# Performance work log

Hardware: AMD Instinct MI355X
Metric: run time of the kernel (lower is better)

## Reference

```python
import jax, jax.numpy as jnp
import numpy as np

B, L, D, K = 16, 2048, 128, 8192
NUM_RQ_STEPS = 1


def _nearest(residual, codebook):
    # residual: [B,L,D], codebook: [K,D]
    d2 = (
        jnp.sum(residual * residual, axis=-1, keepdims=True)  # [B,L,1]
        - 2.0 * jnp.einsum('bld,kd->blk', residual, codebook)  # [B,L,K]
        + jnp.sum(codebook * codebook, axis=-1)  # [K]
    )
    idx = jnp.argmin(d2, axis=-1)  # [B,L]
    return codebook[idx], idx  # gather: [B,L,D]


def setup_inputs() -> dict:
    key = jax.random.key(0)
    k1, k2 = jax.random.split(key)
    z_e = jax.random.normal(k1, (B, L, D), dtype=jnp.float32)
    codebook = jax.random.normal(k2, (K, D), dtype=jnp.float32)
    return {"z_e": z_e, "codebook": codebook}


def reference(z_e, codebook):
    # apply_codebook(z_e, code_sg=True): codebook is stop-gradiented,
    # residual quantization over NUM_RQ_STEPS, straight-through on output.
    cb = jax.lax.stop_gradient(codebook)
    residual = z_e
    z_q = jnp.zeros_like(z_e)
    idx_list = []
    for _ in range(NUM_RQ_STEPS):
        q, idx = _nearest(residual, cb)
        z_q = z_q + q
        residual = residual - q
        idx_list.append(idx)
    indices = jnp.stack(idx_list, axis=-1)  # [B,L,num_rq_steps]
    # straight-through estimator (code_sg=True): grads flow to z_e, not codebook
    z_q = z_e + jax.lax.stop_gradient(z_q - z_e)
    return z_q, indices
```

## Files before the change

### kernel.cpp

```cpp
#include <hip/hip_runtime.h>


#define M_TOK  32768
#define DIM    128
#define KCODES 8192
#define BM     64
#define NT     (KCODES / 256)
#define MARGIN 0.10f
#define RTG    8

typedef _Float16 half8v __attribute__((ext_vector_type(8)));
typedef float float4v __attribute__((ext_vector_type(4)));

union H2U { _Float16 h; unsigned short u; };
__device__ __forceinline__ unsigned short f2h_bits(_Float16 h) {
  H2U c; c.h = h; return c.u;
}

__device__ __forceinline__ void gload_lds16(const void* g, void* l) {
  __builtin_amdgcn_global_load_lds(
      (const __attribute__((address_space(1))) unsigned int*)g,
      (__attribute__((address_space(3))) unsigned int*)l, 16, 0, 0);
}

#define CONSUME_SLICE(P, CNTTXT)                                       \
  do {                                                                 \
    asm volatile("s_waitcnt vmcnt(" CNTTXT ")" ::: "memory");          \
    __builtin_amdgcn_sched_barrier(0);                                 \
    half8v bf[4];                                                      \
    _Pragma("unroll") for (int j_ = 0; j_ < 4; ++j_)                   \
      bf[j_] = *(const half8v*)(BsW + (P) * 4096 + boff[j_]);          \
    _Pragma("unroll") for (int i_ = 0; i_ < 4; ++i_)                   \
      _Pragma("unroll") for (int j_ = 0; j_ < 4; ++j_)                 \
        acc[i_][j_] = __builtin_amdgcn_mfma_f32_16x16x32_f16(          \
            ahi[P][i_], bf[j_], acc[i_][j_], 0, 0, 0);                 \
  } while (0)

#define CNORM_OFF  (KCODES * 256)
#define QCNT_OFF   (CNORM_OFF + KCODES * 4)
#define QTOK_OFF   (QCNT_OFF + 64)
#define KMIN_OFF   (QTOK_OFF + M_TOK * 4)

__global__ __launch_bounds__(256) void prep_kernel(
    const float* __restrict__ cb, unsigned short* __restrict__ Cs,
    float* __restrict__ cnorm, int* __restrict__ qcnt) {
  if (blockIdx.x == 0 && threadIdx.x == 0) *qcnt = 0;
  const int k = blockIdx.x * 4 + (threadIdx.x >> 6);
  const int lane = threadIdx.x & 63;
  const float2 v = ((const float2*)(cb + (size_t)k * DIM))[lane];
  float s = v.x * v.x + v.y * v.y;
  #pragma unroll
  for (int off = 32; off > 0; off >>= 1) s += __shfl_down(s, off);
  if (lane == 0) cnorm[k] = s;
  ushort2 hi;
  hi.x = f2h_bits((_Float16)v.x);
  hi.y = f2h_bits((_Float16)v.y);
  *(ushort2*)(Cs + (size_t)k * 128 + lane * 2) = hi;
}

__global__ __launch_bounds__(256, 2) void vq_mfma_kernel(
    const float* __restrict__ ze, const unsigned short* __restrict__ Cs,
    const float* __restrict__ cnorm, const float* __restrict__ cb,
    int* __restrict__ qcnt, int* __restrict__ qtok,
    unsigned long long* __restrict__ kmin,
    float* __restrict__ out_zq, float* __restrict__ out_idx) {
  __shared__ char lds[65536];
  char* const As = lds;

  const int tid = threadIdx.x;
  const int wn = tid >> 6;
  const int lane = tid & 63;
  const int quad = lane >> 4;
  const int l15 = lane & 15;
  const int m0 = blockIdx.x * BM;

  int loffC[4];
  #pragma unroll
  for (int c = 0; c < 4; ++c) {
    const int r = c * 16 + (lane >> 2);
    const int s = lane & 3;
    const int seg = s ^ ((r >> 1) & 3);
    loffC[c] = (wn * 64 + r) * 256 + seg * 16;
  }
  int boff[4];
  #pragma unroll
  for (int j = 0; j < 4; ++j) {
    const int n = j * 16 + l15;
    boff[j] = n * 64 + ((quad ^ ((n >> 1) & 3)) << 4);
  }
  char* const BsW = lds + wn * 16384;

  {
    const int r = tid >> 2;
    const int qh = tid & 3;
    const float* zrow = ze + (size_t)(m0 + r) * DIM + qh * 32;
    char* arow = As + r * 256;
    const int rx = r & 7;
    #pragma unroll
    for (int i = 0; i < 8; ++i) {
      const float4 v = *(const float4*)(zrow + i * 4);
      ushort4 hh;
      hh.x = f2h_bits((_Float16)v.x);
      hh.y = f2h_bits((_Float16)v.y);
      hh.z = f2h_bits((_Float16)v.z);
      hh.w = f2h_bits((_Float16)v.w);
      const int c = qh * 32 + i * 4;
      *(ushort4*)(arow + ((((c >> 3) ^ rx) << 4) | ((c & 7) << 1))) = hh;
    }
  }
  __syncthreads();

  half8v ahi[4][4];
  #pragma unroll
  for (int ks = 0; ks < 4; ++ks)
    #pragma unroll
    for (int i = 0; i < 4; ++i) {
      const int m = i * 16 + l15;
      const int kslot = ks * 4 + quad;
      ahi[ks][i] = *(const half8v*)(As + m * 256 + ((kslot ^ (m & 7)) << 4));
    }
  __syncthreads();

  float bestv[16], secv[16], idxv[16];
  #pragma unroll
  for (int s = 0; s < 16; ++s) {
    bestv[s] = -3.4e38f; secv[s] = -3.4e38f; idxv[s] = 0.f;
  }

  for (int nt = 0; nt < NT; ++nt) {
    const char* const tile = (const char*)Cs + (size_t)nt * 65536;
    float cnv[4];
    #pragma unroll
    for (int j = 0; j < 4; ++j)
      cnv[j] = cnorm[nt * 256 + wn * 64 + j * 16 + l15];

    float4v acc[4][4];
    #pragma unroll
    for (int i = 0; i < 4; ++i)
      #pragma unroll
      for (int j = 0; j < 4; ++j) acc[i][j] = (float4v)0.0f;

    asm volatile("s_waitcnt lgkmcnt(0)" ::: "memory");
    __builtin_amdgcn_sched_barrier(0);
    #pragma unroll
    for (int p = 0; p < 4; ++p)
      #pragma unroll
      for (int c = 0; c < 4; ++c)
        gload_lds16(tile + p * 64 + loffC[c], BsW + p * 4096 + c * 1024);

    CONSUME_SLICE(0, "12");
    CONSUME_SLICE(1, "8");
    CONSUME_SLICE(2, "4");
    CONSUME_SLICE(3, "0");

    #pragma unroll
    for (int j = 0; j < 4; ++j) {
      const float nidx = (float)(nt * 256 + wn * 64 + j * 16 + l15);
      const float cn = cnv[j];
      #pragma unroll
      for (int i = 0; i < 4; ++i)
        #pragma unroll
        for (int rg = 0; rg < 4; ++rg) {
          const float sc = fmaf(-0.5f, cn, acc[i][j][rg]);
          const int slot = i * 4 + rg;
          const bool bt = sc > bestv[slot];
          secv[slot] = __builtin_amdgcn_fmed3f(sc, bestv[slot], secv[slot]);
          idxv[slot] = bt ? nidx : idxv[slot];
          bestv[slot] = fmaxf(bestv[slot], sc);
        }
    }
  }

  #pragma unroll
  for (int slot = 0; slot < 16; ++slot) {
    float b = bestv[slot], sec = secv[slot], ix = idxv[slot];
    #pragma unroll
    for (int mk = 1; mk <= 8; mk <<= 1) {
      const float ob = __shfl_xor(b, mk);
      const float os = __shfl_xor(sec, mk);
      const float oi = __shfl_xor(ix, mk);
      const bool take = (ob > b) || (ob == b && oi < ix);
      const float loser = take ? b : ob;
      b = take ? ob : b;
      ix = take ? oi : ix;
      sec = fmaxf(fmaxf(sec, os), loser);
    }
    bestv[slot] = b; secv[slot] = sec; idxv[slot] = ix;
  }

  __syncthreads();
  float* const redB = (float*)lds;
  float* const redS = redB + 256;
  float* const redI = redB + 512;
  float* const lidxs = redB + 768;
  if (l15 == 0) {
    #pragma unroll
    for (int slot = 0; slot < 16; ++slot) {
      const int row = (slot >> 2) * 16 + quad * 4 + (slot & 3);
      redB[wn * 64 + row] = bestv[slot];
      redS[wn * 64 + row] = secv[slot];
      redI[wn * 64 + row] = idxv[slot];
    }
  }
  __syncthreads();
  if (tid < 64) {
    float b = redB[tid], sec = redS[tid], ix = redI[tid];
    #pragma unroll
    for (int w = 1; w < 4; ++w) {
      const float ob = redB[w * 64 + tid];
      const float os = redS[w * 64 + tid];
      const float oi = redI[w * 64 + tid];
      const bool take = (ob > b) || (ob == b && oi < ix);
      const float loser = take ? b : ob;
      b = take ? ob : b;
      ix = take ? oi : ix;
      sec = fmaxf(fmaxf(sec, os), loser);
    }
    out_idx[m0 + tid] = ix;
    lidxs[tid] = ix;
    if (b - sec < 0.5f * MARGIN) {
      kmin[m0 + tid] = ~0ull;
      const int p = atomicAdd(qcnt, 1);
      qtok[p] = m0 + tid;
    }
  }
  __syncthreads();

  const int tl = tid >> 2, qp = tid & 3;
  const int code = (int)lidxs[tl];
  const float4* src = (const float4*)(cb + (size_t)code * DIM);
  float4* dst = (float4*)(out_zq + (size_t)(m0 + tl) * DIM);
  #pragma unroll
  for (int p = 0; p < 8; ++p) dst[qp + p * 4] = src[qp + p * 4];
}

__global__ __launch_bounds__(256) void rescan_part_kernel(
    const float* __restrict__ ze, const float* __restrict__ cb,
    const float* __restrict__ cnorm, const int* __restrict__ qcnt,
    const int* __restrict__ qtok, unsigned long long* __restrict__ kmin) {
  __shared__ float xsh[RTG][132];
  __shared__ unsigned long long wpart[4][RTG];
  const int tid = threadIdx.x;
  const int wv = tid >> 6;
  const int lane = tid & 63;
  const int cg = blockIdx.x & 7;
  const int n = *qcnt;
  const int nslots = gridDim.x >> 3;
  const int c0 = cg * 1024 + tid;

  for (int g = blockIdx.x >> 3; g * RTG < n; g += nslots) {
    const int cnt = min(RTG, n - g * RTG);
    __syncthreads();
    if ((tid >> 5) < cnt) {
      const int token = qtok[g * RTG + (tid >> 5)];
      const float4 v =
          ((const float4*)(ze + (size_t)token * DIM))[tid & 31];
      ((float4*)(xsh[tid >> 5]))[tid & 31] = v;
    }
    __syncthreads();

    float dot[4][RTG];
    #pragma unroll
    for (int k = 0; k < 4; ++k)
      #pragma unroll
      for (int t = 0; t < RTG; ++t) dot[k][t] = 0.f;

    const float* crow0 = cb + (size_t)c0 * DIM;
    for (int d = 0; d < DIM; d += 4) {
      float4 x4[RTG];
      #pragma unroll
      for (int t = 0; t < RTG; ++t)
        x4[t] = *(const float4*)(xsh[t] + d);
      #pragma unroll
      for (int k = 0; k < 4; ++k) {
        const float4 c4 = *(const float4*)(crow0 + (size_t)k * 256 * DIM + d);
        #pragma unroll
        for (int t = 0; t < RTG; ++t) {
          dot[k][t] = fmaf(c4.x, x4[t].x, dot[k][t]);
          dot[k][t] = fmaf(c4.y, x4[t].y, dot[k][t]);
          dot[k][t] = fmaf(c4.z, x4[t].z, dot[k][t]);
          dot[k][t] = fmaf(c4.w, x4[t].w, dot[k][t]);
        }
      }
    }

    float cn[4];
    #pragma unroll
    for (int k = 0; k < 4; ++k) cn[k] = cnorm[c0 + k * 256];

    #pragma unroll
    for (int t = 0; t < RTG; ++t) {
      float s = fmaf(-2.f, dot[0][t], cn[0]);
      int ix = c0;
      #pragma unroll
      for (int k = 1; k < 4; ++k) {
        const float sk = fmaf(-2.f, dot[k][t], cn[k]);
        if (sk < s) { s = sk; ix = c0 + k * 256; }
      }
      #pragma unroll
      for (int mk = 1; mk <= 32; mk <<= 1) {
        const float os = __shfl_xor(s, mk);
        const int oi = __shfl_xor(ix, mk);
        if (os < s || (os == s && oi < ix)) { s = os; ix = oi; }
      }
      if (lane == 0) {
        union { float f; unsigned u; } c; c.f = s;
        const unsigned m = (c.u >> 31) ? ~c.u : (c.u | 0x80000000u);
        wpart[wv][t] = ((unsigned long long)m << 32) | (unsigned)ix;
      }
    }
    __syncthreads();
    if (tid < cnt) {
      unsigned long long k = wpart[0][tid];
      #pragma unroll
      for (int w = 1; w < 4; ++w) k = min(k, wpart[w][tid]);
      atomicMin(&kmin[qtok[g * RTG + tid]], k);
    }
  }
}

__global__ __launch_bounds__(256) void rescan_apply_kernel(
    const float* __restrict__ cb, const int* __restrict__ qcnt,
    const int* __restrict__ qtok, const unsigned long long* __restrict__ kmin,
    float* __restrict__ out_zq, float* __restrict__ out_idx) {
  const int tid = threadIdx.x;
  const int n = *qcnt;
  for (int qi = blockIdx.x; qi < n; qi += gridDim.x) {
    const int token = qtok[qi];
    const int code = (int)(unsigned int)(kmin[token] & 0xFFFFFFFFull);
    if (tid == 0) out_idx[token] = (float)code;
    if (tid < 32)
      ((float4*)(out_zq + (size_t)token * DIM))[tid] =
          ((const float4*)(cb + (size_t)code * DIM))[tid];
  }
}

extern "C" void kernel_launch(void* const* d_in, const int* in_sizes, int n_in,
                              void* d_out, int out_size, void* d_ws,
                              size_t ws_size, hipStream_t stream) {
  const float* ze = (const float*)d_in[0];
  const float* cb = (const float*)d_in[1];
  float* out = (float*)d_out;

  unsigned short* Cs = (unsigned short*)d_ws;
  float* cnorm = (float*)((char*)d_ws + CNORM_OFF);
  int* qcnt = (int*)((char*)d_ws + QCNT_OFF);
  int* qtok = (int*)((char*)d_ws + QTOK_OFF);
  unsigned long long* kmin = (unsigned long long*)((char*)d_ws + KMIN_OFF);

  prep_kernel<<<KCODES / 4, 256, 0, stream>>>(cb, Cs, cnorm, qcnt);
  vq_mfma_kernel<<<M_TOK / BM, 256, 0, stream>>>(
      ze, Cs, cnorm, cb, qcnt, qtok, kmin, out, out + (size_t)M_TOK * DIM);
  rescan_part_kernel<<<4096, 256, 0, stream>>>(ze, cb, cnorm, qcnt, qtok,
                                               kmin);
  rescan_apply_kernel<<<256, 256, 0, stream>>>(cb, qcnt, qtok, kmin, out,
                                               out + (size_t)M_TOK * DIM);
}
```

Baseline: 248.9 us.

## Software-pipeline codebook tile loads to prefetch the next tile during MFMA

Restructures the codebook tile loop so that the global-to-LDS loads for tile nt+1 go out as soon as the matching slices of tile nt have been consumed. The next tile's cnorm values are prefetched into registers, and the final tile is peeled out of the loop. The aim is to hide global load latency behind the MFMA work and the argmax fold, which used to wait on a cold load at the start of every tile. The tighter vmcnt bookkeeping and the removed lgkmcnt(0) wait before overwriting LDS slices add a risk of read/write hazards on the reused buffer.

```diff
diff --git a/kernel.cpp b/kernel.cpp
--- a/kernel.cpp
+++ b/kernel.cpp
@@ -36,6 +36,32 @@
             ahi[P][i_], bf[j_], acc[i_][j_], 0, 0, 0);                 \
   } while (0)
 
+#define STAGE_SLICE(TB, P)                                             \
+  do {                                                                 \
+    _Pragma("unroll") for (int c_ = 0; c_ < 4; ++c_)                   \
+      gload_lds16((TB) + (P) * 64 + loffC[c_],                         \
+                  BsW + (P) * 4096 + c_ * 1024);                       \
+  } while (0)
+
+#define FOLD_TILE(NTV, CNV)                                            \
+  do {                                                                 \
+    _Pragma("unroll") for (int j_ = 0; j_ < 4; ++j_) {                 \
+      const float nidx_ =                                              \
+          (float)((NTV) * 256 + wn * 64 + j_ * 16 + l15);              \
+      const float cn_ = (CNV)[j_];                                     \
+      _Pragma("unroll") for (int i_ = 0; i_ < 4; ++i_)                 \
+        _Pragma("unroll") for (int rg_ = 0; rg_ < 4; ++rg_) {          \
+          const float sc_ = fmaf(-0.5f, cn_, acc[i_][j_][rg_]);        \
+          const int slot_ = i_ * 4 + rg_;                              \
+          const bool bt_ = sc_ > bestv[slot_];                         \
+          secv[slot_] =                                                \
+              __builtin_amdgcn_fmed3f(sc_, bestv[slot_], secv[slot_]); \
+          idxv[slot_] = bt_ ? nidx_ : idxv[slot_];                     \
+          bestv[slot_] = fmaxf(bestv[slot_], sc_);                     \
+        }                                                              \
+    }                                                                  \
+  } while (0)
+
 #define CNORM_OFF  (KCODES * 256)
 #define QCNT_OFF   (CNORM_OFF + KCODES * 4)
 #define QTOK_OFF   (QCNT_OFF + 64)
@@ -127,48 +153,58 @@
     bestv[s] = -3.4e38f; secv[s] = -3.4e38f; idxv[s] = 0.f;
   }
 
-  for (int nt = 0; nt < NT; ++nt) {
-    const char* const tile = (const char*)Cs + (size_t)nt * 65536;
-    float cnv[4];
+  float cnv[4];
+  #pragma unroll
+  for (int j = 0; j < 4; ++j)
+    cnv[j] = cnorm[wn * 64 + j * 16 + l15];
+  {
+    const char* const t0 = (const char*)Cs;
+    STAGE_SLICE(t0, 0); STAGE_SLICE(t0, 1);
+    STAGE_SLICE(t0, 2); STAGE_SLICE(t0, 3);
+  }
+
+  for (int nt = 0; nt < NT - 1; ++nt) {
+    float4v acc[4][4];
+    #pragma unroll
+    for (int i = 0; i < 4; ++i)
+      #pragma unroll
+      for (int j = 0; j < 4; ++j) acc[i][j] = (float4v)0.0f;
+
+    CONSUME_SLICE(0, "12");
+    CONSUME_SLICE(1, "8");
+    __builtin_amdgcn_sched_barrier(0);
+
+    float cnvn[4];
     #pragma unroll
     for (int j = 0; j < 4; ++j)
-      cnv[j] = cnorm[nt * 256 + wn * 64 + j * 16 + l15];
-
+      cnvn[j] = cnorm[(nt + 1) * 256 + wn * 64 + j * 16 + l15];
+    const char* const tnext = (const char*)Cs + (size_t)(nt + 1) * 65536;
+    STAGE_SLICE(tnext, 0);
+    STAGE_SLICE(tnext, 1);
+
+    CONSUME_SLICE(2, "16");
+    CONSUME_SLICE(3, "12");
+    __builtin_amdgcn_sched_barrier(0);
+
+    STAGE_SLICE(tnext, 2);
+    STAGE_SLICE(tnext, 3);
+
+    FOLD_TILE(nt, cnv);
+    #pragma unroll
+    for (int j = 0; j < 4; ++j) cnv[j] = cnvn[j];
+  }
+
+  {
     float4v acc[4][4];
     #pragma unroll
     for (int i = 0; i < 4; ++i)
       #pragma unroll
       for (int j = 0; j < 4; ++j) acc[i][j] = (float4v)0.0f;
-
-    asm volatile("s_waitcnt lgkmcnt(0)" ::: "memory");
-    __builtin_amdgcn_sched_barrier(0);
-    #pragma unroll
-    for (int p = 0; p < 4; ++p)
-      #pragma unroll
-      for (int c = 0; c < 4; ++c)
-        gload_lds16(tile + p * 64 + loffC[c], BsW + p * 4096 + c * 1024);
-
     CONSUME_SLICE(0, "12");
     CONSUME_SLICE(1, "8");
     CONSUME_SLICE(2, "4");
     CONSUME_SLICE(3, "0");
-
-    #pragma unroll
-    for (int j = 0; j < 4; ++j) {
-      const float nidx = (float)(nt * 256 + wn * 64 + j * 16 + l15);
-      const float cn = cnv[j];
-      #pragma unroll
-      for (int i = 0; i < 4; ++i)
-        #pragma unroll
-        for (int rg = 0; rg < 4; ++rg) {
-          const float sc = fmaf(-0.5f, cn, acc[i][j][rg]);
-          const int slot = i * 4 + rg;
-          const bool bt = sc > bestv[slot];
-          secv[slot] = __builtin_amdgcn_fmed3f(sc, bestv[slot], secv[slot]);
-          idxv[slot] = bt ? nidx : idxv[slot];
-          bestv[slot] = fmaxf(bestv[slot], sc);
-        }
-    }
+    FOLD_TILE(NT - 1, cnv);
   }
 
   #pragma unroll
```

New measurement: 248.8 us. About the same (-0.0%).
